# Kernel tuning notes

Measured on AMD Instinct MI355X. Metric: run time of the kernel, lower is better.

The kernel has to match this reference:

```python
import jax, jax.numpy as jnp
import numpy as np

T, B, D_IN, D_H = 1024, 128, 256, 256


def setup_inputs() -> dict:
    key = jax.random.key(0)
    ks = jax.random.split(key, 9)
    s_in = 1.0 / np.sqrt(D_IN + D_H)  # torch nn.Linear init scale
    inputs = jax.random.normal(ks[0], (T, B, D_IN), dtype=jnp.float32)
    def lin(kw, kb):
        W = jax.random.uniform(kw, (D_IN + D_H, D_H), jnp.float32, -s_in, s_in)
        b = jax.random.uniform(kb, (D_H,), jnp.float32, -s_in, s_in)
        return W, b
    Wf, bf = lin(ks[1], ks[2])
    Wi, bi = lin(ks[3], ks[4])
    Wg, bg = lin(ks[5], ks[6])
    Wo, bo = lin(ks[7], ks[8])
    return {"inputs": inputs, "Wf": Wf, "bf": bf, "Wi": Wi, "bi": bi,
            "Wg": Wg, "bg": bg, "Wo": Wo, "bo": bo}


def reference(inputs, Wf, bf, Wi, bi, Wg, bg, Wo, bo):
    Bsz = inputs.shape[1]
    h0 = jnp.zeros((Bsz, D_H), inputs.dtype)
    c0 = jnp.zeros((Bsz, D_H), inputs.dtype)

    def step(carry, x):
        hx, cx = carry
        combined = jnp.concatenate([x, hx], axis=1)  # [B, D_IN+D_H]
        f = jax.nn.sigmoid(combined @ Wf + bf)
        i = jax.nn.sigmoid(combined @ Wi + bi)
        g = jnp.tanh(combined @ Wg + bg)
        o = jax.nn.sigmoid(combined @ Wo + bo)
        cx = f * cx + i * g
        hx = o * jnp.tanh(cx)
        return (hx, cx), hx

    (hx, cx), outputs = jax.lax.scan(step, (h0, c0), inputs)
    return outputs, (hx, cx)
```

## Files before the change

### kernel.cpp

```cpp
#include <hip/hip_runtime.h>
#include <hip/hip_bf16.h>

typedef short s16x8 __attribute__((ext_vector_type(8)));
typedef int   i32x4 __attribute__((ext_vector_type(4)));
typedef float f32x4 __attribute__((ext_vector_type(4)));
typedef float f32x2 __attribute__((ext_vector_type(2)));

#define T_STEPS 1024
#define BATCH   128
#define DIN     256
#define DH      256
#define NWG     64
#define NTHREADS 256

static __device__ __forceinline__ short f2bf(float f) {
  return __builtin_bit_cast(short, (__bf16)f);
}
static __device__ __forceinline__ float sigf(float x){ return 1.f/(1.f+__expf(-x)); }
static __device__ __forceinline__ float tanhfast(float x){ return 1.f - 2.f/(1.f+__expf(2.f*x)); }

static __device__ __forceinline__ i32x4 ld16_cc(const void* p){
  i32x4 r; asm volatile("global_load_dwordx4 %0, %1, off sc0 sc1" : "=v"(r) : "v"(p) : "memory"); return r;
}
static __device__ __forceinline__ unsigned ld4_cc(const void* p){
  unsigned r; asm volatile("global_load_dword %0, %1, off sc0 sc1\ns_waitcnt vmcnt(0)" : "=v"(r) : "v"(p) : "memory"); return r;
}
static __device__ __forceinline__ void st4_cc(void* p, unsigned v){
  asm volatile("global_store_dword %0, %1, off sc0 sc1" :: "v"(p), "v"(v) : "memory");
}

static __device__ __forceinline__ s16x8 cvt8(f32x4 a, f32x4 b){
  s16x8 r;
  r[0]=f2bf(a[0]); r[1]=f2bf(a[1]); r[2]=f2bf(a[2]); r[3]=f2bf(a[3]);
  r[4]=f2bf(b[0]); r[5]=f2bf(b[1]); r[6]=f2bf(b[2]); r[7]=f2bf(b[3]);
  return r;
}

__global__ __launch_bounds__(NTHREADS, 1)
void lstm_rc(const float* __restrict__ X,
             const float* __restrict__ Wf, const float* __restrict__ bfv,
             const float* __restrict__ Wi, const float* __restrict__ biv,
             const float* __restrict__ Wg, const float* __restrict__ bgv,
             const float* __restrict__ Wo, const float* __restrict__ bov,
             float* __restrict__ out,
             unsigned short* __restrict__ hbuf,
             unsigned int* __restrict__ flags,
             int needEnd)
{
  const int bid = blockIdx.x;
  const int r   = bid & 7;
  const int csl = bid >> 3;
  const int tid = threadIdx.x;
  const int lane = tid & 63, wv = tid >> 6;
  const int grp = lane >> 4, l15 = lane & 15;
  const int r0 = r * 16;

  __shared__ short bfx[64 * 64 * 8];
  __shared__ float elds[4 * 16 * 36];

  s16x8 bh[2][8];
  {
    const float* Wm[4] = {Wf, Wi, Wg, Wo};
    const int gate = l15 >> 2, jj = l15 & 3;
    const float* Wsrc = Wm[gate];
#pragma unroll
    for (int n2 = 0; n2 < 2; ++n2) {
      const int hc = csl * 32 + (wv * 2 + n2) * 4 + jj;
#pragma unroll
      for (int kk = 0; kk < 16; ++kk) {
        const float* p = Wsrc + (size_t)(kk * 32 + grp * 8) * DH + hc;
        s16x8 f;
#pragma unroll
        for (int s = 0; s < 8; ++s) f[s] = f2bf(p[(size_t)s * DH]);
        if (kk < 8) *(s16x8*)&bfx[(((wv * 2 + n2) * 8 + kk) * 64 + lane) * 8] = f;
        else        bh[n2][kk - 8] = f;
      }
    }
  }

  const int colg = csl * 32 + wv * 8 + 2 * grp;
  float bia[4][2];
  {
    const float* Bv[4] = {bfv, biv, bgv, bov};
#pragma unroll
    for (int g = 0; g < 4; ++g) { bia[g][0] = Bv[g][colg]; bia[g][1] = Bv[g][colg + 1]; }
  }
  __syncthreads();

  f32x4 xr[16];
  {
    const float* xs0 = X + (size_t)(r0 + l15) * DIN + grp * 8;
#pragma unroll
    for (int kk = 0; kk < 8; ++kk) {
      xr[2 * kk]     = *(const f32x4*)(xs0 + kk * 32);
      xr[2 * kk + 1] = *(const f32x4*)(xs0 + kk * 32 + 4);
    }
  }
  f32x4 accx0 = {0.f,0.f,0.f,0.f}, accx1 = {0.f,0.f,0.f,0.f};
#pragma unroll
  for (int kk = 0; kk < 8; ++kk) {
    s16x8 fa = cvt8(xr[2 * kk], xr[2 * kk + 1]);
    s16x8 b0 = *(const s16x8*)&bfx[(((wv * 2 + 0) * 8 + kk) * 64 + lane) * 8];
    s16x8 b1 = *(const s16x8*)&bfx[(((wv * 2 + 1) * 8 + kk) * 64 + lane) * 8];
    accx0 = __builtin_amdgcn_mfma_f32_16x16x32_bf16(fa, b0, accx0, 0, 0, 0);
    accx1 = __builtin_amdgcn_mfma_f32_16x16x32_bf16(fa, b1, accx1, 0, 0, 0);
  }

  unsigned* myflag = flags + (r * 32 + csl);
  const unsigned* pollp = flags + (r * 32 + (lane & 7));
  float* eldsw = &elds[wv * 16 * 36];
  float cs0 = 0.f, cs1 = 0.f, h0s = 0.f, h1s = 0.f;

  for (int t = 0; t < T_STEPS; ++t) {
    while (1) {
      unsigned v = ld4_cc(pollp);
      if (__all((int)(v >= (unsigned)t))) break;
    }
    __builtin_amdgcn_sched_barrier(0);

    const unsigned short* hr = hbuf + (size_t)(t & 1) * (BATCH * DH)
                             + (size_t)(r0 + l15) * DH + grp * 8;
    i32x4 hraw[8];
#pragma unroll
    for (int q = 0; q < 8; ++q) hraw[q] = ld16_cc(hr + q * 32);
    asm volatile("s_waitcnt vmcnt(0)" ::: "memory");
    __builtin_amdgcn_sched_barrier(0);

    f32x4 acc0 = accx0, acc1 = accx1;
#pragma unroll
    for (int q = 0; q < 8; ++q) {
      s16x8 ah = __builtin_bit_cast(s16x8, hraw[q]);
      acc0 = __builtin_amdgcn_mfma_f32_16x16x32_bf16(ah, bh[0][q], acc0, 0, 0, 0);
      acc1 = __builtin_amdgcn_mfma_f32_16x16x32_bf16(ah, bh[1][q], acc1, 0, 0, 0);
    }

#pragma unroll
    for (int rr = 0; rr < 4; ++rr) {
      eldsw[(grp * 4 + rr) * 36 + l15]      = acc0[rr];
      eldsw[(grp * 4 + rr) * 36 + 16 + l15] = acc1[rr];
    }
    asm volatile("s_waitcnt lgkmcnt(0)" ::: "memory");
    __builtin_amdgcn_sched_barrier(0);
    float z0[4], z1[4];
    const int hc0 = 2 * grp, hc1 = 2 * grp + 1;
#pragma unroll
    for (int g = 0; g < 4; ++g) {
      z0[g] = eldsw[l15 * 36 + ((hc0 >> 2) << 4) + 4 * g + (hc0 & 3)];
      z1[g] = eldsw[l15 * 36 + ((hc1 >> 2) << 4) + 4 * g + (hc1 & 3)];
    }

    {
      float zf = z0[0] + bia[0][0], zi = z0[1] + bia[1][0];
      float zg = z0[2] + bia[2][0], zo = z0[3] + bia[3][0];
      cs0 = sigf(zf) * cs0 + sigf(zi) * tanhfast(zg);
      h0s = sigf(zo) * tanhfast(cs0);
    }
    {
      float zf = z1[0] + bia[0][1], zi = z1[1] + bia[1][1];
      float zg = z1[2] + bia[2][1], zo = z1[3] + bia[3][1];
      cs1 = sigf(zf) * cs1 + sigf(zi) * tanhfast(zg);
      h1s = sigf(zo) * tanhfast(cs1);
    }

    const int row = r0 + l15;
    {
      unsigned hpk = (unsigned)(unsigned short)f2bf(h0s)
                   | ((unsigned)(unsigned short)f2bf(h1s) << 16);
      st4_cc(hbuf + (size_t)((t + 1) & 1) * (BATCH * DH)
             + (size_t)row * DH + colg, hpk);
    }
    asm volatile("s_waitcnt vmcnt(0)" ::: "memory");
    __syncthreads();
    if (tid == 0) st4_cc(myflag, (unsigned)(t + 1));

    {
      f32x2 ov; ov[0] = h0s; ov[1] = h1s;
      *(f32x2*)(out + ((size_t)t * BATCH + row) * DH + colg) = ov;
    }
    {
      const int tnx = (t + 1 < T_STEPS) ? t + 1 : T_STEPS - 1;
      const float* xs = X + ((size_t)tnx * BATCH + r0 + l15) * DIN + grp * 8;
#pragma unroll
      for (int kk = 0; kk < 8; ++kk) {
        xr[2 * kk]     = *(const f32x4*)(xs + kk * 32);
        xr[2 * kk + 1] = *(const f32x4*)(xs + kk * 32 + 4);
      }
    }
    accx0 = (f32x4){0.f,0.f,0.f,0.f}; accx1 = (f32x4){0.f,0.f,0.f,0.f};
#pragma unroll
    for (int kk = 0; kk < 8; ++kk) {
      s16x8 fa = cvt8(xr[2 * kk], xr[2 * kk + 1]);
      s16x8 b0 = *(const s16x8*)&bfx[(((wv * 2 + 0) * 8 + kk) * 64 + lane) * 8];
      s16x8 b1 = *(const s16x8*)&bfx[(((wv * 2 + 1) * 8 + kk) * 64 + lane) * 8];
      accx0 = __builtin_amdgcn_mfma_f32_16x16x32_bf16(fa, b0, accx0, 0, 0, 0);
      accx1 = __builtin_amdgcn_mfma_f32_16x16x32_bf16(fa, b1, accx1, 0, 0, 0);
    }
  }

  if (needEnd) {
    if (wv == 0) {
      const unsigned* fp = flags + ((lane >> 3) * 32 + (lane & 7));
      while (ld4_cc(fp) < (unsigned)T_STEPS) __builtin_amdgcn_s_sleep(1);
    }
    __syncthreads();
  }
  {
    const size_t base = (size_t)T_STEPS * BATCH * DH;
    const size_t idx  = (size_t)(r0 + l15) * DH + colg;
    out[base + idx]     = h0s;
    out[base + idx + 1] = h1s;
    out[base + BATCH * DH + idx]     = cs0;
    out[base + BATCH * DH + idx + 1] = cs1;
  }
}

extern "C" void kernel_launch(void* const* d_in, const int* in_sizes, int n_in,
                              void* d_out, int out_size, void* d_ws, size_t ws_size,
                              hipStream_t stream) {
  const float* X   = (const float*)d_in[0];
  const float* Wf  = (const float*)d_in[1];
  const float* bf_ = (const float*)d_in[2];
  const float* Wi  = (const float*)d_in[3];
  const float* bi_ = (const float*)d_in[4];
  const float* Wg  = (const float*)d_in[5];
  const float* bg_ = (const float*)d_in[6];
  const float* Wo  = (const float*)d_in[7];
  const float* bo_ = (const float*)d_in[8];
  float* out = (float*)d_out;

  const size_t hbytes = (size_t)2 * BATCH * DH * 2;
  const size_t fbytes = 2048;
  unsigned short* hbuf;
  unsigned int*   flags;
  int needEnd;
  if (ws_size >= hbytes + fbytes) {
    hbuf  = (unsigned short*)d_ws;
    flags = (unsigned int*)((unsigned char*)d_ws + hbytes);
    needEnd = 0;
    hipMemsetAsync(d_ws, 0, hbytes + fbytes, stream);
  } else {
    unsigned char* tail = (unsigned char*)d_out + (size_t)T_STEPS * BATCH * DH * 4;
    hbuf  = (unsigned short*)tail;
    flags = (unsigned int*)(tail + hbytes);
    needEnd = 1;
    hipMemsetAsync(tail, 0, hbytes + fbytes, stream);
  }

  lstm_rc<<<NWG, NTHREADS, 0, stream>>>(X, Wf, bf_, Wi, bi_, Wg, bg_,
                                        Wo, bo_, out, hbuf, flags, needEnd);
}
```

Baseline: 4.414 ms.

## Interleave two independent batch halves per workgroup to hide cross-block sync latency

Halves the grid to 32 workgroups, each handling two 16-row batch slices (A and B) whose recurrences are independent, so the wait on one slice's flags overlaps with compute on the other. Synchronisation moves from a per-block __syncthreads plus one flag to per-wave flags polled by 32 lanes. The input projection is staged as bf16 into double-buffered LDS, with X prefetched two steps ahead. Each workgroup does twice the MFMA work per step, and the two-phase ordering adds complexity to the memory-ordering logic.

```diff
diff --git a/kernel.cpp b/kernel.cpp
--- a/kernel.cpp
+++ b/kernel.cpp
@@ -10,52 +10,57 @@
 #define BATCH   128
 #define DIN     256
 #define DH      256
-#define NWG     64
+#define NWG     32
 #define NTHREADS 256
 
-static __device__ __forceinline__ short f2bf(float f) {
-  return __builtin_bit_cast(short, (__bf16)f);
+static __device__ __forceinline__ short f2bf(float f){ return __builtin_bit_cast(short,(__bf16)f); }
+static __device__ __forceinline__ float sigf(float x){ return 1.f/(1.f+__expf(-x)); }
+static __device__ __forceinline__ float tanhfast(float x){ return 1.f-2.f/(1.f+__expf(2.f*x)); }
+
+static __device__ __forceinline__ i32x4 ld16_cc_i(const void* p){ i32x4 r; asm volatile("global_load_dwordx4 %0, %1, off sc0 sc1" : "=v"(r) : "v"(p) : "memory"); return r; }
+static __device__ __forceinline__ i32x4 ld16_pl_i(const void* p){ i32x4 r; asm volatile("global_load_dwordx4 %0, %1, off" : "=v"(r) : "v"(p) : "memory"); return r; }
+static __device__ __forceinline__ unsigned ld4_cc_i(const void* p){ unsigned r; asm volatile("global_load_dword %0, %1, off sc0 sc1" : "=v"(r) : "v"(p) : "memory"); return r; }
+static __device__ __forceinline__ unsigned ld4_cc_w(const void* p){ unsigned r; asm volatile("global_load_dword %0, %1, off sc0 sc1\ns_waitcnt vmcnt(0)" : "=v"(r) : "v"(p) : "memory"); return r; }
+static __device__ __forceinline__ void st4_cc_i(void* p, unsigned v){ asm volatile("global_store_dword %0, %1, off sc0 sc1" :: "v"(p), "v"(v) : "memory"); }
+static __device__ __forceinline__ void st8_pl_i(void* p, f32x2 v){ asm volatile("global_store_dwordx2 %0, %1, off" :: "v"(p), "v"(v) : "memory"); }
+#define VMW(n)  asm volatile("s_waitcnt vmcnt(" #n ")" ::: "memory")
+#define LGKM0   asm volatile("s_waitcnt lgkmcnt(0)" ::: "memory")
+#define SCHED0  __builtin_amdgcn_sched_barrier(0)
+#define POLLWAIT(val, ptr, tgt) \
+  while (!__all((int)((val) >= (unsigned)(tgt)))) { (val) = ld4_cc_w(ptr); }
+
+static __device__ __forceinline__ void stageX(short* dst, int xseg, int xrow,
+                                              f32x4 a, f32x4 b, f32x4 c, f32x4 d){
+  s16x8 lo, hi;
+  lo[0]=f2bf(a[0]); lo[1]=f2bf(a[1]); lo[2]=f2bf(a[2]); lo[3]=f2bf(a[3]);
+  lo[4]=f2bf(b[0]); lo[5]=f2bf(b[1]); lo[6]=f2bf(b[2]); lo[7]=f2bf(b[3]);
+  hi[0]=f2bf(c[0]); hi[1]=f2bf(c[1]); hi[2]=f2bf(c[2]); hi[3]=f2bf(c[3]);
+  hi[4]=f2bf(d[0]); hi[5]=f2bf(d[1]); hi[6]=f2bf(d[2]); hi[7]=f2bf(d[3]);
+  *(s16x8*)&dst[((2*xseg+0)*16 + xrow)*8] = lo;
+  *(s16x8*)&dst[((2*xseg+1)*16 + xrow)*8] = hi;
 }
-static __device__ __forceinline__ float sigf(float x){ return 1.f/(1.f+__expf(-x)); }
-static __device__ __forceinline__ float tanhfast(float x){ return 1.f - 2.f/(1.f+__expf(2.f*x)); }
-
-static __device__ __forceinline__ i32x4 ld16_cc(const void* p){
-  i32x4 r; asm volatile("global_load_dwordx4 %0, %1, off sc0 sc1" : "=v"(r) : "v"(p) : "memory"); return r;
-}
-static __device__ __forceinline__ unsigned ld4_cc(const void* p){
-  unsigned r; asm volatile("global_load_dword %0, %1, off sc0 sc1\ns_waitcnt vmcnt(0)" : "=v"(r) : "v"(p) : "memory"); return r;
-}
-static __device__ __forceinline__ void st4_cc(void* p, unsigned v){
-  asm volatile("global_store_dword %0, %1, off sc0 sc1" :: "v"(p), "v"(v) : "memory");
-}
-
-static __device__ __forceinline__ s16x8 cvt8(f32x4 a, f32x4 b){
-  s16x8 r;
-  r[0]=f2bf(a[0]); r[1]=f2bf(a[1]); r[2]=f2bf(a[2]); r[3]=f2bf(a[3]);
-  r[4]=f2bf(b[0]); r[5]=f2bf(b[1]); r[6]=f2bf(b[2]); r[7]=f2bf(b[3]);
-  return r;
-}
 
 __global__ __launch_bounds__(NTHREADS, 1)
-void lstm_rc(const float* __restrict__ X,
-             const float* __restrict__ Wf, const float* __restrict__ bfv,
-             const float* __restrict__ Wi, const float* __restrict__ biv,
-             const float* __restrict__ Wg, const float* __restrict__ bgv,
-             const float* __restrict__ Wo, const float* __restrict__ bov,
-             float* __restrict__ out,
-             unsigned short* __restrict__ hbuf,
-             unsigned int* __restrict__ flags,
-             int needEnd)
+void lstm_pipe(const float* __restrict__ X,
+               const float* __restrict__ Wf, const float* __restrict__ bfv,
+               const float* __restrict__ Wi, const float* __restrict__ biv,
+               const float* __restrict__ Wg, const float* __restrict__ bgv,
+               const float* __restrict__ Wo, const float* __restrict__ bov,
+               float* __restrict__ out,
+               unsigned short* __restrict__ hbuf,
+               unsigned int* __restrict__ flags,
+               int needEnd)
 {
   const int bid = blockIdx.x;
-  const int r   = bid & 7;
-  const int csl = bid >> 3;
+  const int g   = bid & 3;
+  const int csl = bid >> 2;
   const int tid = threadIdx.x;
   const int lane = tid & 63, wv = tid >> 6;
   const int grp = lane >> 4, l15 = lane & 15;
-  const int r0 = r * 16;
+  const int r0A = g * 32, r0B = g * 32 + 16;
 
   __shared__ short bfx[64 * 64 * 8];
+  __shared__ short axl[4 * 32 * 16 * 8];
   __shared__ float elds[4 * 16 * 36];
 
   s16x8 bh[2][8];
@@ -83,134 +88,225 @@
   {
     const float* Bv[4] = {bfv, biv, bgv, bov};
 #pragma unroll
-    for (int g = 0; g < 4; ++g) { bia[g][0] = Bv[g][colg]; bia[g][1] = Bv[g][colg + 1]; }
+    for (int q = 0; q < 4; ++q) { bia[q][0] = Bv[q][colg]; bia[q][1] = Bv[q][colg + 1]; }
   }
   __syncthreads();
 
-  f32x4 xr[16];
-  {
-    const float* xs0 = X + (size_t)(r0 + l15) * DIN + grp * 8;
-#pragma unroll
-    for (int kk = 0; kk < 8; ++kk) {
-      xr[2 * kk]     = *(const f32x4*)(xs0 + kk * 32);
-      xr[2 * kk + 1] = *(const f32x4*)(xs0 + kk * 32 + 4);
-    }
-  }
-  f32x4 accx0 = {0.f,0.f,0.f,0.f}, accx1 = {0.f,0.f,0.f,0.f};
-#pragma unroll
-  for (int kk = 0; kk < 8; ++kk) {
-    s16x8 fa = cvt8(xr[2 * kk], xr[2 * kk + 1]);
-    s16x8 b0 = *(const s16x8*)&bfx[(((wv * 2 + 0) * 8 + kk) * 64 + lane) * 8];
-    s16x8 b1 = *(const s16x8*)&bfx[(((wv * 2 + 1) * 8 + kk) * 64 + lane) * 8];
-    accx0 = __builtin_amdgcn_mfma_f32_16x16x32_bf16(fa, b0, accx0, 0, 0, 0);
-    accx1 = __builtin_amdgcn_mfma_f32_16x16x32_bf16(fa, b1, accx1, 0, 0, 0);
-  }
-
-  unsigned* myflag = flags + (r * 32 + csl);
-  const unsigned* pollp = flags + (r * 32 + (lane & 7));
+  const int xrow = tid & 15, xseg = tid >> 4;
+  {
+    const float* xsA = X + (size_t)(r0A + xrow) * DIN + xseg * 16;
+    stageX(axl + 0 * (32 * 16 * 8), xseg, xrow,
+           *(const f32x4*)xsA, *(const f32x4*)(xsA + 4),
+           *(const f32x4*)(xsA + 8), *(const f32x4*)(xsA + 12));
+    const float* xsB = X + (size_t)(r0B + xrow) * DIN + xseg * 16;
+    stageX(axl + 2 * (32 * 16 * 8), xseg, xrow,
+           *(const f32x4*)xsB, *(const f32x4*)(xsB + 4),
+           *(const f32x4*)(xsB + 8), *(const f32x4*)(xsB + 12));
+  }
+  __syncthreads();
+
+  const unsigned* pollA = flags + (g * 2 + 0) * 32 + (lane & 31);
+  const unsigned* pollB = flags + (g * 2 + 1) * 32 + (lane & 31);
+  unsigned* flagAw = flags + (g * 2 + 0) * 32 + csl * 4 + wv;
+  unsigned* flagBw = flags + (g * 2 + 1) * 32 + csl * 4 + wv;
   float* eldsw = &elds[wv * 16 * 36];
-  float cs0 = 0.f, cs1 = 0.f, h0s = 0.f, h1s = 0.f;
+
+  f32x4 xra[4], xrb[4];
+  {
+    const float* xs = X + ((size_t)1 * BATCH + r0A + xrow) * DIN + xseg * 16;
+    xra[0] = __builtin_bit_cast(f32x4, ld16_pl_i(xs));
+    xra[1] = __builtin_bit_cast(f32x4, ld16_pl_i(xs + 4));
+    xra[2] = __builtin_bit_cast(f32x4, ld16_pl_i(xs + 8));
+    xra[3] = __builtin_bit_cast(f32x4, ld16_pl_i(xs + 12));
+  }
+  unsigned pav = ld4_cc_i(pollA), pbv;
+  {
+    const float* xs = X + ((size_t)1 * BATCH + r0B + xrow) * DIN + xseg * 16;
+    xrb[0] = __builtin_bit_cast(f32x4, ld16_pl_i(xs));
+    xrb[1] = __builtin_bit_cast(f32x4, ld16_pl_i(xs + 4));
+    xrb[2] = __builtin_bit_cast(f32x4, ld16_pl_i(xs + 8));
+    xrb[3] = __builtin_bit_cast(f32x4, ld16_pl_i(xs + 12));
+  }
+
+  float csA0 = 0.f, csA1 = 0.f, hA0v = 0.f, hA1v = 0.f;
+  float csB0 = 0.f, csB1 = 0.f, hB0v = 0.f, hB1v = 0.f;
 
   for (int t = 0; t < T_STEPS; ++t) {
-    while (1) {
-      unsigned v = ld4_cc(pollp);
-      if (__all((int)(v >= (unsigned)t))) break;
-    }
-    __builtin_amdgcn_sched_barrier(0);
-
-    const unsigned short* hr = hbuf + (size_t)(t & 1) * (BATCH * DH)
-                             + (size_t)(r0 + l15) * DH + grp * 8;
-    i32x4 hraw[8];
-#pragma unroll
-    for (int q = 0; q < 8; ++q) hraw[q] = ld16_cc(hr + q * 32);
-    asm volatile("s_waitcnt vmcnt(0)" ::: "memory");
-    __builtin_amdgcn_sched_barrier(0);
-
-    f32x4 acc0 = accx0, acc1 = accx1;
+    const int pr = t & 1, pw = (t + 1) & 1;
+
+    VMW(4); SCHED0;
+    POLLWAIT(pav, pollA, t);
+    SCHED0;
+
+    pbv = ld4_cc_i(pollB);
+    const unsigned short* hrA = hbuf + (size_t)pr * (BATCH * DH)
+                              + (size_t)(r0A + l15) * DH + grp * 8;
+    i32x4 ha[8];
+#pragma unroll
+    for (int q = 0; q < 8; ++q) ha[q] = ld16_cc_i(hrA + q * 32);
+
+    f32x4 a0 = {0.f,0.f,0.f,0.f}, a1 = {0.f,0.f,0.f,0.f};
+    {
+      const short* ab = axl + (0 * 2 + pr) * (32 * 16 * 8);
+#pragma unroll
+      for (int kk = 0; kk < 8; ++kk) {
+        s16x8 a  = *(const s16x8*)&ab[((kk * 4 + grp) * 16 + l15) * 8];
+        s16x8 b0 = *(const s16x8*)&bfx[(((wv * 2 + 0) * 8 + kk) * 64 + lane) * 8];
+        s16x8 b1 = *(const s16x8*)&bfx[(((wv * 2 + 1) * 8 + kk) * 64 + lane) * 8];
+        a0 = __builtin_amdgcn_mfma_f32_16x16x32_bf16(a, b0, a0, 0, 0, 0);
+        a1 = __builtin_amdgcn_mfma_f32_16x16x32_bf16(a, b1, a1, 0, 0, 0);
+      }
+    }
+
+    VMW(0); SCHED0;
+    POLLWAIT(pbv, pollB, t);
+    SCHED0;
+
+    const unsigned short* hrB = hbuf + (size_t)pr * (BATCH * DH)
+                              + (size_t)(r0B + l15) * DH + grp * 8;
+    i32x4 hb[8];
+#pragma unroll
+    for (int q = 0; q < 8; ++q) hb[q] = ld16_cc_i(hrB + q * 32);
+
 #pragma unroll
     for (int q = 0; q < 8; ++q) {
-      s16x8 ah = __builtin_bit_cast(s16x8, hraw[q]);
-      acc0 = __builtin_amdgcn_mfma_f32_16x16x32_bf16(ah, bh[0][q], acc0, 0, 0, 0);
-      acc1 = __builtin_amdgcn_mfma_f32_16x16x32_bf16(ah, bh[1][q], acc1, 0, 0, 0);
+      s16x8 ah = __builtin_bit_cast(s16x8, ha[q]);
+      a0 = __builtin_amdgcn_mfma_f32_16x16x32_bf16(ah, bh[0][q], a0, 0, 0, 0);
+      a1 = __builtin_amdgcn_mfma_f32_16x16x32_bf16(ah, bh[1][q], a1, 0, 0, 0);
     }
 
 #pragma unroll
     for (int rr = 0; rr < 4; ++rr) {
-      eldsw[(grp * 4 + rr) * 36 + l15]      = acc0[rr];
-      eldsw[(grp * 4 + rr) * 36 + 16 + l15] = acc1[rr];
-    }
-    asm volatile("s_waitcnt lgkmcnt(0)" ::: "memory");
-    __builtin_amdgcn_sched_barrier(0);
-    float z0[4], z1[4];
-    const int hc0 = 2 * grp, hc1 = 2 * grp + 1;
-#pragma unroll
-    for (int g = 0; g < 4; ++g) {
-      z0[g] = eldsw[l15 * 36 + ((hc0 >> 2) << 4) + 4 * g + (hc0 & 3)];
-      z1[g] = eldsw[l15 * 36 + ((hc1 >> 2) << 4) + 4 * g + (hc1 & 3)];
-    }
-
-    {
+      eldsw[(grp * 4 + rr) * 36 + l15]      = a0[rr];
+      eldsw[(grp * 4 + rr) * 36 + 16 + l15] = a1[rr];
+    }
+    LGKM0; SCHED0;
+    {
+      const int hc0 = 2 * grp, hc1 = 2 * grp + 1;
+      float z0[4], z1[4];
+#pragma unroll
+      for (int q = 0; q < 4; ++q) {
+        z0[q] = eldsw[l15 * 36 + ((hc0 >> 2) << 4) + 4 * q + (hc0 & 3)];
+        z1[q] = eldsw[l15 * 36 + ((hc1 >> 2) << 4) + 4 * q + (hc1 & 3)];
+      }
       float zf = z0[0] + bia[0][0], zi = z0[1] + bia[1][0];
       float zg = z0[2] + bia[2][0], zo = z0[3] + bia[3][0];
-      cs0 = sigf(zf) * cs0 + sigf(zi) * tanhfast(zg);
-      h0s = sigf(zo) * tanhfast(cs0);
-    }
-    {
-      float zf = z1[0] + bia[0][1], zi = z1[1] + bia[1][1];
-      float zg = z1[2] + bia[2][1], zo = z1[3] + bia[3][1];
-      cs1 = sigf(zf) * cs1 + sigf(zi) * tanhfast(zg);
-      h1s = sigf(zo) * tanhfast(cs1);
-    }
-
-    const int row = r0 + l15;
-    {
-      unsigned hpk = (unsigned)(unsigned short)f2bf(h0s)
-                   | ((unsigned)(unsigned short)f2bf(h1s) << 16);
-      st4_cc(hbuf + (size_t)((t + 1) & 1) * (BATCH * DH)
-             + (size_t)row * DH + colg, hpk);
-    }
-    asm volatile("s_waitcnt vmcnt(0)" ::: "memory");
+      csA0 = sigf(zf) * csA0 + sigf(zi) * tanhfast(zg);
+      hA0v = sigf(zo) * tanhfast(csA0);
+      zf = z1[0] + bia[0][1]; zi = z1[1] + bia[1][1];
+      zg = z1[2] + bia[2][1]; zo = z1[3] + bia[3][1];
+      csA1 = sigf(zf) * csA1 + sigf(zi) * tanhfast(zg);
+      hA1v = sigf(zo) * tanhfast(csA1);
+    }
+
+    {
+      unsigned hpk = (unsigned)(unsigned short)f2bf(hA0v)
+                   | ((unsigned)(unsigned short)f2bf(hA1v) << 16);
+      st4_cc_i(hbuf + (size_t)pw * (BATCH * DH) + (size_t)(r0A + l15) * DH + colg, hpk);
+      f32x2 ov; ov[0] = hA0v; ov[1] = hA1v;
+      st8_pl_i(out + ((size_t)t * BATCH + (r0A + l15)) * DH + colg, ov);
+    }
+
+    stageX(axl + (0 * 2 + pw) * (32 * 16 * 8), xseg, xrow, xra[0], xra[1], xra[2], xra[3]);
+    LGKM0;
+
+    VMW(1); SCHED0;
+    if (lane == 0) st4_cc_i(flagAw, (unsigned)(t + 1));
+
+    {
+      const int tp = (t + 2 < T_STEPS) ? t + 2 : T_STEPS - 1;
+      const float* xs = X + ((size_t)tp * BATCH + r0A + xrow) * DIN + xseg * 16;
+      xra[0] = __builtin_bit_cast(f32x4, ld16_pl_i(xs));
+      xra[1] = __builtin_bit_cast(f32x4, ld16_pl_i(xs + 4));
+      xra[2] = __builtin_bit_cast(f32x4, ld16_pl_i(xs + 8));
+      xra[3] = __builtin_bit_cast(f32x4, ld16_pl_i(xs + 12));
+    }
+
+    f32x4 b0 = {0.f,0.f,0.f,0.f}, b1 = {0.f,0.f,0.f,0.f};
+    {
+      const short* ab = axl + (1 * 2 + pr) * (32 * 16 * 8);
+#pragma unroll
+      for (int kk = 0; kk < 8; ++kk) {
+        s16x8 a  = *(const s16x8*)&ab[((kk * 4 + grp) * 16 + l15) * 8];
+        s16x8 bb0 = *(const s16x8*)&bfx[(((wv * 2 + 0) * 8 + kk) * 64 + lane) * 8];
+        s16x8 bb1 = *(const s16x8*)&bfx[(((wv * 2 + 1) * 8 + kk) * 64 + lane) * 8];
+        b0 = __builtin_amdgcn_mfma_f32_16x16x32_bf16(a, bb0, b0, 0, 0, 0);
+        b1 = __builtin_amdgcn_mfma_f32_16x16x32_bf16(a, bb1, b1, 0, 0, 0);
+      }
+    }
+#pragma unroll
+    for (int q = 0; q < 8; ++q) {
+      s16x8 ah = __builtin_bit_cast(s16x8, hb[q]);
+      b0 = __builtin_amdgcn_mfma_f32_16x16x32_bf16(ah, bh[0][q], b0, 0, 0, 0);
+      b1 = __builtin_amdgcn_mfma_f32_16x16x32_bf16(ah, bh[1][q], b1, 0, 0, 0);
+    }
+
+#pragma unroll
+    for (int rr = 0; rr < 4; ++rr) {
+      eldsw[(grp * 4 + rr) * 36 + l15]      = b0[rr];
+      eldsw[(grp * 4 + rr) * 36 + 16 + l15] = b1[rr];
+    }
+    LGKM0; SCHED0;
+    {
+      const int hc0 = 2 * grp, hc1 = 2 * grp + 1;
+      float z0[4], z1[4];
+#pragma unroll
+      for (int q = 0; q < 4; ++q) {
+        z0[q] = eldsw[l15 * 36 + ((hc0 >> 2) << 4) + 4 * q + (hc0 & 3)];
+        z1[q] = eldsw[l15 * 36 + ((hc1 >> 2) << 4) + 4 * q + (hc1 & 3)];
+      }
+      float zf = z0[0] + bia[0][0], zi = z0[1] + bia[1][0];
+      float zg = z0[2] + bia[2][0], zo = z0[3] + bia[3][0];
+      csB0 = sigf(zf) * csB0 + sigf(zi) * tanhfast(zg);
+      hB0v = sigf(zo) * tanhfast(csB0);
+      zf = z1[0] + bia[0][1]; zi = z1[1] + bia[1][1];
+      zg = z1[2] + bia[2][1]; zo = z1[3] + bia[3][1];
+      csB1 = sigf(zf) * csB1 + sigf(zi) * tanhfast(zg);
+      hB1v = sigf(zo) * tanhfast(csB1);
+    }
+
+    {
+      unsigned hpk = (unsigned)(unsigned short)f2bf(hB0v)
+                   | ((unsigned)(unsigned short)f2bf(hB1v) << 16);
+      st4_cc_i(hbuf + (size_t)pw * (BATCH * DH) + (size_t)(r0B + l15) * DH + colg, hpk);
+      f32x2 ov; ov[0] = hB0v; ov[1] = hB1v;
+      st8_pl_i(out + ((size_t)t * BATCH + (r0B + l15)) * DH + colg, ov);
+    }
+
+    stageX(axl + (1 * 2 + pw) * (32 * 16 * 8), xseg, xrow, xrb[0], xrb[1], xrb[2], xrb[3]);
+    LGKM0;
+
+    VMW(1); SCHED0;
+    if (lane == 0) st4_cc_i(flagBw, (unsigned)(t + 1));
+
+    pav = ld4_cc_i(pollA);
+    {
+      const int tp = (t + 2 < T_STEPS) ? t + 2 : T_STEPS - 1;
+      const float* xs = X + ((size_t)tp * BATCH + r0B + xrow) * DIN + xseg * 16;
+      xrb[0] = __builtin_bit_cast(f32x4, ld16_pl_i(xs));
+      xrb[1] = __builtin_bit_cast(f32x4, ld16_pl_i(xs + 4));
+      xrb[2] = __builtin_bit_cast(f32x4, ld16_pl_i(xs + 8));
+      xrb[3] = __builtin_bit_cast(f32x4, ld16_pl_i(xs + 12));
+    }
+  }
+
+  if (needEnd) {
+    const unsigned* fp = flags + tid;
+    while (ld4_cc_w(fp) < (unsigned)T_STEPS) __builtin_amdgcn_s_sleep(1);
     __syncthreads();
-    if (tid == 0) st4_cc(myflag, (unsigned)(t + 1));
-
-    {
-      f32x2 ov; ov[0] = h0s; ov[1] = h1s;
-      *(f32x2*)(out + ((size_t)t * BATCH + row) * DH + colg) = ov;
-    }
-    {
-      const int tnx = (t + 1 < T_STEPS) ? t + 1 : T_STEPS - 1;
-      const float* xs = X + ((size_t)tnx * BATCH + r0 + l15) * DIN + grp * 8;
-#pragma unroll
-      for (int kk = 0; kk < 8; ++kk) {
-        xr[2 * kk]     = *(const f32x4*)(xs + kk * 32);
-        xr[2 * kk + 1] = *(const f32x4*)(xs + kk * 32 + 4);
-      }
-    }
-    accx0 = (f32x4){0.f,0.f,0.f,0.f}; accx1 = (f32x4){0.f,0.f,0.f,0.f};
-#pragma unroll
-    for (int kk = 0; kk < 8; ++kk) {
-      s16x8 fa = cvt8(xr[2 * kk], xr[2 * kk + 1]);
-      s16x8 b0 = *(const s16x8*)&bfx[(((wv * 2 + 0) * 8 + kk) * 64 + lane) * 8];
-      s16x8 b1 = *(const s16x8*)&bfx[(((wv * 2 + 1) * 8 + kk) * 64 + lane) * 8];
-      accx0 = __builtin_amdgcn_mfma_f32_16x16x32_bf16(fa, b0, accx0, 0, 0, 0);
-      accx1 = __builtin_amdgcn_mfma_f32_16x16x32_bf16(fa, b1, accx1, 0, 0, 0);
-    }
-  }
-
-  if (needEnd) {
-    if (wv == 0) {
-      const unsigned* fp = flags + ((lane >> 3) * 32 + (lane & 7));
-      while (ld4_cc(fp) < (unsigned)T_STEPS) __builtin_amdgcn_s_sleep(1);
-    }
-    __syncthreads();
   }
   {
     const size_t base = (size_t)T_STEPS * BATCH * DH;
-    const size_t idx  = (size_t)(r0 + l15) * DH + colg;
-    out[base + idx]     = h0s;
-    out[base + idx + 1] = h1s;
-    out[base + BATCH * DH + idx]     = cs0;
-    out[base + BATCH * DH + idx + 1] = cs1;
+    const size_t idxA = (size_t)(r0A + l15) * DH + colg;
+    const size_t idxB = (size_t)(r0B + l15) * DH + colg;
+    out[base + idxA]     = hA0v;
+    out[base + idxA + 1] = hA1v;
+    out[base + BATCH * DH + idxA]     = csA0;
+    out[base + BATCH * DH + idxA + 1] = csA1;
+    out[base + idxB]     = hB0v;
+    out[base + idxB + 1] = hB1v;
+    out[base + BATCH * DH + idxB]     = csB0;
+    out[base + BATCH * DH + idxB + 1] = csB1;
   }
 }
 
@@ -246,6 +342,6 @@
     hipMemsetAsync(tail, 0, hbytes + fbytes, stream);
   }
 
-  lstm_rc<<<NWG, NTHREADS, 0, stream>>>(X, Wf, bf_, Wi, bi_, Wg, bg_,
-                                        Wo, bo_, out, hbuf, flags, needEnd);
+  lstm_pipe<<<NWG, NTHREADS, 0, stream>>>(X, Wf, bf_, Wi, bi_, Wg, bg_,
+                                          Wo, bo_, out, hbuf, flags, needEnd);
 }
```

Measured after the change: 4.261 ms. 1.04x faster.

## Split LSTM batch across independent workgroups streaming prepacked bf16 weights

Applied to the files above, without the earlier changes.

Replaces the 64-workgroup kernel, which synchronises every timestep through global flags, with 16 independent workgroups of 512 threads. Each workgroup owns 8 batch rows and keeps h and x in LDS, so no cross-workgroup synchronisation is needed. Weights are prepacked once into MFMA fragment layout in bf16 by a separate kernel. Every timestep then streams all weights (1 MB per workgroup) from L2/global through a triple-buffered register pipeline. This trades inter-WG flag latency for heavy repeated weight bandwidth, and only half of each 16-row MFMA tile holds real batch rows. The new path is used only when the workspace is at least 1 MB.

```diff
diff --git a/kernel.cpp b/kernel.cpp
--- a/kernel.cpp
+++ b/kernel.cpp
@@ -2,6 +2,7 @@
 #include <hip/hip_bf16.h>
 
 typedef short s16x8 __attribute__((ext_vector_type(8)));
+typedef short s16x4 __attribute__((ext_vector_type(4)));
 typedef int   i32x4 __attribute__((ext_vector_type(4)));
 typedef float f32x4 __attribute__((ext_vector_type(4)));
 typedef float f32x2 __attribute__((ext_vector_type(2)));
@@ -10,14 +11,190 @@
 #define BATCH   128
 #define DIN     256
 #define DH      256
-#define NWG     64
-#define NTHREADS 256
-
-static __device__ __forceinline__ short f2bf(float f) {
-  return __builtin_bit_cast(short, (__bf16)f);
-}
+
+static __device__ __forceinline__ short f2bf(float f){ return __builtin_bit_cast(short,(__bf16)f); }
 static __device__ __forceinline__ float sigf(float x){ return 1.f/(1.f+__expf(-x)); }
-static __device__ __forceinline__ float tanhfast(float x){ return 1.f - 2.f/(1.f+__expf(2.f*x)); }
+static __device__ __forceinline__ float tanhfast(float x){ return 1.f-2.f/(1.f+__expf(2.f*x)); }
+
+__global__ void build_frags(const float* __restrict__ Wf, const float* __restrict__ Wi,
+                            const float* __restrict__ Wg, const float* __restrict__ Wo,
+                            unsigned short* __restrict__ frag) {
+  const float* Wm[4] = {Wf, Wi, Wg, Wo};
+  int p0 = blockIdx.x * 256 + threadIdx.x;
+#pragma unroll
+  for (int i = 0; i < 4; ++i) {
+    int p = p0 + i * 16384;
+    int lane = p & 63;
+    int F = p >> 6;
+    int kk = F & 15, gate = (F >> 4) & 3, b = (F >> 6) & 1, w = F >> 7;
+    int k0 = kk * 32 + (lane >> 4) * 8;
+    int col = w * 32 + b * 16 + (lane & 15);
+    const float* src = Wm[gate] + (size_t)k0 * DH + col;
+    unsigned short* dst = frag + (size_t)p * 8;
+#pragma unroll
+    for (int s = 0; s < 8; ++s) dst[s] = (unsigned short)f2bf(src[(size_t)s * DH]);
+  }
+}
+
+#define LDF(dst, base, OFF) \
+  asm volatile("global_load_dwordx4 %0, %1, off offset:" #OFF : "=v"(dst) : "v"(base) : "memory")
+#define WAITV(N) do { asm volatile("s_waitcnt vmcnt(" #N ")" ::: "memory"); \
+  __builtin_amdgcn_sched_barrier(0); } while (0)
+
+#define HALF_ISSUE(B) do { \
+  LDF(bq[B][0], fwp, 0); LDF(bq[B][1], fwp, 1024); \
+  LDF(bq[B][2], fwp, 2048); LDF(bq[B][3], fwp, 3072); \
+  LDF(bq[B][4], fwp2, 0); LDF(bq[B][5], fwp2, 1024); \
+  LDF(bq[B][6], fwp2, 2048); LDF(bq[B][7], fwp2, 3072); \
+  fwp += 8192; fwp2 += 8192; } while (0)
+
+#define HALF_MFMA(B, AARR, BI, GI) do { \
+  acc[BI][GI] = __builtin_amdgcn_mfma_f32_16x16x32_bf16(AARR[0], __builtin_bit_cast(s16x8, bq[B][0]), acc[BI][GI], 0,0,0); \
+  acc[BI][GI] = __builtin_amdgcn_mfma_f32_16x16x32_bf16(AARR[1], __builtin_bit_cast(s16x8, bq[B][1]), acc[BI][GI], 0,0,0); \
+  acc[BI][GI] = __builtin_amdgcn_mfma_f32_16x16x32_bf16(AARR[2], __builtin_bit_cast(s16x8, bq[B][2]), acc[BI][GI], 0,0,0); \
+  acc[BI][GI] = __builtin_amdgcn_mfma_f32_16x16x32_bf16(AARR[3], __builtin_bit_cast(s16x8, bq[B][3]), acc[BI][GI], 0,0,0); \
+  acc[BI][GI] = __builtin_amdgcn_mfma_f32_16x16x32_bf16(AARR[4], __builtin_bit_cast(s16x8, bq[B][4]), acc[BI][GI], 0,0,0); \
+  acc[BI][GI] = __builtin_amdgcn_mfma_f32_16x16x32_bf16(AARR[5], __builtin_bit_cast(s16x8, bq[B][5]), acc[BI][GI], 0,0,0); \
+  acc[BI][GI] = __builtin_amdgcn_mfma_f32_16x16x32_bf16(AARR[6], __builtin_bit_cast(s16x8, bq[B][6]), acc[BI][GI], 0,0,0); \
+  acc[BI][GI] = __builtin_amdgcn_mfma_f32_16x16x32_bf16(AARR[7], __builtin_bit_cast(s16x8, bq[B][7]), acc[BI][GI], 0,0,0); } while (0)
+
+#define EPI(BI, CBX) do { \
+  _Pragma("unroll") \
+  for (int r = 0; r < 4; ++r) { \
+    float zf = acc[BI][0][r] + bia[0][BI]; \
+    float zi = acc[BI][1][r] + bia[1][BI]; \
+    float zg = acc[BI][2][r] + bia[2][BI]; \
+    float zo = acc[BI][3][r] + bia[3][BI]; \
+    float cn = sigf(zf) * cs[BI][r] + sigf(zi) * tanhfast(zg); \
+    cs[BI][r] = cn; \
+    float hv = sigf(zo) * tanhfast(cn); \
+    hq[BI][r] = hv; \
+    if (grp < 2) HL[pw * 4352 + (grp * 4 + r) * 272 + (CBX)] = (unsigned short)f2bf(hv); \
+  } } while (0)
+
+__global__ __launch_bounds__(512, 2)
+void lstm_cu(const float* __restrict__ X,
+             const float* __restrict__ bfv, const float* __restrict__ biv,
+             const float* __restrict__ bgv, const float* __restrict__ bov,
+             const unsigned short* __restrict__ frag,
+             float* __restrict__ out)
+{
+  const int tid = threadIdx.x;
+  const int lane = tid & 63, w = tid >> 6;
+  const int grp = lane >> 4, l15 = lane & 15;
+  const int g8 = blockIdx.x * 8;
+
+  __shared__ unsigned short XL[2 * 16 * 272];
+  __shared__ unsigned short HL[2 * 16 * 272];
+
+  for (int i = tid; i < 2 * 16 * 272; i += 512) { XL[i] = 0; HL[i] = 0; }
+
+  const int cb0 = w * 32 + l15, cb1 = w * 32 + 16 + l15;
+  float bia[4][2];
+  {
+    const float* Bv[4] = {bfv, biv, bgv, bov};
+#pragma unroll
+    for (int g = 0; g < 4; ++g) { bia[g][0] = Bv[g][cb0]; bia[g][1] = Bv[g][cb1]; }
+  }
+
+  const int xr = tid >> 6, xc = (tid & 63) * 4;
+
+  {
+    f32x4 v = *(const f32x4*)(X + ((size_t)0 * BATCH + g8 + xr) * DIN + xc);
+    s16x4 h4; h4[0]=f2bf(v[0]); h4[1]=f2bf(v[1]); h4[2]=f2bf(v[2]); h4[3]=f2bf(v[3]);
+    *(s16x4*)&XL[0 * 4352 + xr * 272 + xc] = h4;
+  }
+  __syncthreads();
+
+  i32x4 xq;
+  LDF(xq, (const char*)(X + ((size_t)1 * BATCH + g8 + xr) * DIN + xc), 0);
+
+  const char* fragw = (const char*)frag + (size_t)w * 131072;
+  float cs[2][4] = {{0,0,0,0},{0,0,0,0}};
+  float hq[2][4] = {{0,0,0,0},{0,0,0,0}};
+
+  for (int t = 0; t < T_STEPS; ++t) {
+    const int pr = t & 1, pw = pr ^ 1;
+
+    asm volatile("s_waitcnt vmcnt(0)" ::: "memory");
+    __builtin_amdgcn_sched_barrier(0);
+
+    {
+      f32x4 v = __builtin_bit_cast(f32x4, xq);
+      s16x4 h4; h4[0]=f2bf(v[0]); h4[1]=f2bf(v[1]); h4[2]=f2bf(v[2]); h4[3]=f2bf(v[3]);
+      *(s16x4*)&XL[pw * 4352 + xr * 272 + xc] = h4;
+    }
+
+    s16x8 ax[8], ah[8];
+#pragma unroll
+    for (int q = 0; q < 8; ++q) {
+      ax[q] = *(const s16x8*)&XL[pr * 4352 + l15 * 272 + q * 32 + grp * 8];
+      ah[q] = *(const s16x8*)&HL[pr * 4352 + l15 * 272 + q * 32 + grp * 8];
+    }
+
+    f32x4 acc[2][4];
+#pragma unroll
+    for (int b = 0; b < 2; ++b)
+#pragma unroll
+      for (int g = 0; g < 4; ++g) acc[b][g] = (f32x4){0.f,0.f,0.f,0.f};
+
+    i32x4 bq[3][8];
+    const char* fwp  = fragw + lane * 16;
+    const char* fwp2 = fwp + 4096;
+
+    HALF_ISSUE(0); HALF_ISSUE(1);
+    HALF_ISSUE(2); WAITV(16); HALF_MFMA(0, ax, 0, 0);
+    HALF_ISSUE(0); WAITV(16); HALF_MFMA(1, ah, 0, 0);
+    HALF_ISSUE(1); WAITV(16); HALF_MFMA(2, ax, 0, 1);
+    HALF_ISSUE(2); WAITV(16); HALF_MFMA(0, ah, 0, 1);
+    HALF_ISSUE(0); WAITV(16); HALF_MFMA(1, ax, 0, 2);
+    HALF_ISSUE(1); WAITV(16); HALF_MFMA(2, ah, 0, 2);
+    HALF_ISSUE(2); WAITV(16); HALF_MFMA(0, ax, 0, 3);
+    HALF_ISSUE(0); WAITV(16); HALF_MFMA(1, ah, 0, 3);
+    EPI(0, cb0);
+    HALF_ISSUE(1); WAITV(16); HALF_MFMA(2, ax, 1, 0);
+    HALF_ISSUE(2); WAITV(16); HALF_MFMA(0, ah, 1, 0);
+    HALF_ISSUE(0); WAITV(16); HALF_MFMA(1, ax, 1, 1);
+    HALF_ISSUE(1); WAITV(16); HALF_MFMA(2, ah, 1, 1);
+    HALF_ISSUE(2); WAITV(16); HALF_MFMA(0, ax, 1, 2);
+    HALF_ISSUE(0); WAITV(16); HALF_MFMA(1, ah, 1, 2);
+    WAITV(8);  HALF_MFMA(2, ax, 1, 3);
+    WAITV(0);  HALF_MFMA(0, ah, 1, 3);
+
+    {
+      const int tp = (t + 2 < T_STEPS) ? t + 2 : T_STEPS - 1;
+      LDF(xq, (const char*)(X + ((size_t)tp * BATCH + g8 + xr) * DIN + xc), 0);
+    }
+
+    EPI(1, cb1);
+
+    if (grp < 2) {
+      size_t rb = ((size_t)t * BATCH + g8 + grp * 4) * DH;
+#pragma unroll
+      for (int r = 0; r < 4; ++r) {
+        out[rb + (size_t)r * DH + cb0] = hq[0][r];
+        out[rb + (size_t)r * DH + cb1] = hq[1][r];
+      }
+    }
+
+    asm volatile("s_waitcnt lgkmcnt(0)" ::: "memory");
+    __builtin_amdgcn_sched_barrier(0);
+    __builtin_amdgcn_s_barrier();
+    __builtin_amdgcn_sched_barrier(0);
+  }
+
+  if (grp < 2) {
+    const size_t base = (size_t)T_STEPS * BATCH * DH;
+#pragma unroll
+    for (int r = 0; r < 4; ++r) {
+      size_t idx = (size_t)(g8 + grp * 4 + r) * DH;
+      out[base + idx + cb0] = hq[0][r];
+      out[base + idx + cb1] = hq[1][r];
+      out[base + BATCH * DH + idx + cb0] = cs[0][r];
+      out[base + BATCH * DH + idx + cb1] = cs[1][r];
+    }
+  }
+}
 
 static __device__ __forceinline__ i32x4 ld16_cc(const void* p){
   i32x4 r; asm volatile("global_load_dwordx4 %0, %1, off sc0 sc1" : "=v"(r) : "v"(p) : "memory"); return r;
@@ -28,7 +205,6 @@
 static __device__ __forceinline__ void st4_cc(void* p, unsigned v){
   asm volatile("global_store_dword %0, %1, off sc0 sc1" :: "v"(p), "v"(v) : "memory");
 }
-
 static __device__ __forceinline__ s16x8 cvt8(f32x4 a, f32x4 b){
   s16x8 r;
   r[0]=f2bf(a[0]); r[1]=f2bf(a[1]); r[2]=f2bf(a[2]); r[3]=f2bf(a[3]);
@@ -36,16 +212,16 @@
   return r;
 }
 
-__global__ __launch_bounds__(NTHREADS, 1)
-void lstm_rc(const float* __restrict__ X,
-             const float* __restrict__ Wf, const float* __restrict__ bfv,
-             const float* __restrict__ Wi, const float* __restrict__ biv,
-             const float* __restrict__ Wg, const float* __restrict__ bgv,
-             const float* __restrict__ Wo, const float* __restrict__ bov,
-             float* __restrict__ out,
-             unsigned short* __restrict__ hbuf,
-             unsigned int* __restrict__ flags,
-             int needEnd)
+__global__ __launch_bounds__(256, 1)
+void lstm_rc_fb(const float* __restrict__ X,
+                const float* __restrict__ Wf, const float* __restrict__ bfv,
+                const float* __restrict__ Wi, const float* __restrict__ biv,
+                const float* __restrict__ Wg, const float* __restrict__ bgv,
+                const float* __restrict__ Wo, const float* __restrict__ bov,
+                float* __restrict__ out,
+                unsigned short* __restrict__ hbuf,
+                unsigned int* __restrict__ flags,
+                int needEnd)
 {
   const int bid = blockIdx.x;
   const int r   = bid & 7;
@@ -148,7 +324,6 @@
       z0[g] = eldsw[l15 * 36 + ((hc0 >> 2) << 4) + 4 * g + (hc0 & 3)];
       z1[g] = eldsw[l15 * 36 + ((hc1 >> 2) << 4) + 4 * g + (hc1 & 3)];
     }
-
     {
       float zf = z0[0] + bia[0][0], zi = z0[1] + bia[1][0];
       float zg = z0[2] + bia[2][0], zo = z0[3] + bia[3][0];
@@ -161,7 +336,6 @@
       cs1 = sigf(zf) * cs1 + sigf(zi) * tanhfast(zg);
       h1s = sigf(zo) * tanhfast(cs1);
     }
-
     const int row = r0 + l15;
     {
       unsigned hpk = (unsigned)(unsigned short)f2bf(h0s)
@@ -227,6 +401,13 @@
   const float* Wo  = (const float*)d_in[7];
   const float* bo_ = (const float*)d_in[8];
   float* out = (float*)d_out;
+
+  if (ws_size >= (size_t)(1u << 20)) {
+    unsigned short* frag = (unsigned short*)d_ws;
+    build_frags<<<64, 256, 0, stream>>>(Wf, Wi, Wg, Wo, frag);
+    lstm_cu<<<16, 512, 0, stream>>>(X, bf_, bi_, bg_, bo_, frag, out);
+    return;
+  }
 
   const size_t hbytes = (size_t)2 * BATCH * DH * 2;
   const size_t fbytes = 2048;
@@ -245,7 +426,6 @@
     needEnd = 1;
     hipMemsetAsync(tail, 0, hbytes + fbytes, stream);
   }
-
-  lstm_rc<<<NWG, NTHREADS, 0, stream>>>(X, Wf, bf_, Wi, bi_, Wg, bg_,
-                                        Wo, bo_, out, hbuf, flags, needEnd);
-}
+  lstm_rc_fb<<<64, 256, 0, stream>>>(X, Wf, bf_, Wi, bi_, Wg, bg_,
+                                     Wo, bo_, out, hbuf, flags, needEnd);
+}
```

Measured after the change: 12.57 ms. 2.85x slower.

## Replace flag polling with timestep-tagged hidden-state words for inter-block sync

Applied to the files above, without the earlier changes.

Each bf16 hidden value is now stored in a 32-bit word whose upper half carries the timestep tag. Consumers poll the hidden-state data directly until every tag matches the current step. This removes the separate flag write, the vmcnt wait plus __syncthreads before publishing, and the flag-then-data double round trip on the per-step critical path. In exchange each step reads twice as many bytes and retries full loads while spinning, and the old flag path is kept as a fallback when the workspace is too small.

```diff
diff --git a/kernel.cpp b/kernel.cpp
--- a/kernel.cpp
+++ b/kernel.cpp
@@ -3,6 +3,7 @@
 
 typedef short s16x8 __attribute__((ext_vector_type(8)));
 typedef int   i32x4 __attribute__((ext_vector_type(4)));
+typedef unsigned u32x2 __attribute__((ext_vector_type(2)));
 typedef float f32x4 __attribute__((ext_vector_type(4)));
 typedef float f32x2 __attribute__((ext_vector_type(2)));
 
@@ -13,11 +14,9 @@
 #define NWG     64
 #define NTHREADS 256
 
-static __device__ __forceinline__ short f2bf(float f) {
-  return __builtin_bit_cast(short, (__bf16)f);
-}
+static __device__ __forceinline__ short f2bf(float f){ return __builtin_bit_cast(short,(__bf16)f); }
 static __device__ __forceinline__ float sigf(float x){ return 1.f/(1.f+__expf(-x)); }
-static __device__ __forceinline__ float tanhfast(float x){ return 1.f - 2.f/(1.f+__expf(2.f*x)); }
+static __device__ __forceinline__ float tanhfast(float x){ return 1.f-2.f/(1.f+__expf(2.f*x)); }
 
 static __device__ __forceinline__ i32x4 ld16_cc(const void* p){
   i32x4 r; asm volatile("global_load_dwordx4 %0, %1, off sc0 sc1" : "=v"(r) : "v"(p) : "memory"); return r;
@@ -27,6 +26,9 @@
 }
 static __device__ __forceinline__ void st4_cc(void* p, unsigned v){
   asm volatile("global_store_dword %0, %1, off sc0 sc1" :: "v"(p), "v"(v) : "memory");
+}
+static __device__ __forceinline__ void st8_cc(void* p, u32x2 v){
+  asm volatile("global_store_dwordx2 %0, %1, off sc0 sc1" :: "v"(p), "v"(v) : "memory");
 }
 
 static __device__ __forceinline__ s16x8 cvt8(f32x4 a, f32x4 b){
@@ -37,15 +39,13 @@
 }
 
 __global__ __launch_bounds__(NTHREADS, 1)
-void lstm_rc(const float* __restrict__ X,
-             const float* __restrict__ Wf, const float* __restrict__ bfv,
-             const float* __restrict__ Wi, const float* __restrict__ biv,
-             const float* __restrict__ Wg, const float* __restrict__ bgv,
-             const float* __restrict__ Wo, const float* __restrict__ bov,
-             float* __restrict__ out,
-             unsigned short* __restrict__ hbuf,
-             unsigned int* __restrict__ flags,
-             int needEnd)
+void lstm_tag(const float* __restrict__ X,
+              const float* __restrict__ Wf, const float* __restrict__ bfv,
+              const float* __restrict__ Wi, const float* __restrict__ biv,
+              const float* __restrict__ Wg, const float* __restrict__ bgv,
+              const float* __restrict__ Wo, const float* __restrict__ bov,
+              float* __restrict__ out,
+              unsigned* __restrict__ htag)
 {
   const int bid = blockIdx.x;
   const int r   = bid & 7;
@@ -106,6 +106,187 @@
     accx1 = __builtin_amdgcn_mfma_f32_16x16x32_bf16(fa, b1, accx1, 0, 0, 0);
   }
 
+  float cs0 = 0.f, cs1 = 0.f, h0s = 0.f, h1s = 0.f;
+
+  for (int t = 0; t < T_STEPS; ++t) {
+    const unsigned tte = (unsigned)t << 16;
+    const unsigned* hb = htag + (size_t)(t & 1) * (BATCH * DH)
+                       + (size_t)(r0 + l15) * DH + grp * 8;
+    i32x4 hraw[16];
+    while (1) {
+#pragma unroll
+      for (int q = 0; q < 8; ++q) {
+        hraw[2 * q]     = ld16_cc(hb + q * 32);
+        hraw[2 * q + 1] = ld16_cc(hb + q * 32 + 4);
+      }
+      asm volatile("s_waitcnt vmcnt(0)" ::: "memory");
+      unsigned bad = 0;
+#pragma unroll
+      for (int i2 = 0; i2 < 16; ++i2)
+        bad |= (unsigned)(hraw[i2][0] ^ (int)tte) | (unsigned)(hraw[i2][2] ^ (int)tte);
+      bad &= 0xFFFF0000u;
+      if (__all((int)(bad == 0))) break;
+    }
+    __builtin_amdgcn_sched_barrier(0);
+
+    f32x4 acc0 = accx0, acc1 = accx1;
+#pragma unroll
+    for (int q = 0; q < 8; ++q) {
+      i32x4 hp;
+      hp[0] = (int)__builtin_amdgcn_perm((unsigned)hraw[2*q][1],   (unsigned)hraw[2*q][0],   0x05040100u);
+      hp[1] = (int)__builtin_amdgcn_perm((unsigned)hraw[2*q][3],   (unsigned)hraw[2*q][2],   0x05040100u);
+      hp[2] = (int)__builtin_amdgcn_perm((unsigned)hraw[2*q+1][1], (unsigned)hraw[2*q+1][0], 0x05040100u);
+      hp[3] = (int)__builtin_amdgcn_perm((unsigned)hraw[2*q+1][3], (unsigned)hraw[2*q+1][2], 0x05040100u);
+      s16x8 ah = __builtin_bit_cast(s16x8, hp);
+      acc0 = __builtin_amdgcn_mfma_f32_16x16x32_bf16(ah, bh[0][q], acc0, 0, 0, 0);
+      acc1 = __builtin_amdgcn_mfma_f32_16x16x32_bf16(ah, bh[1][q], acc1, 0, 0, 0);
+    }
+
+#pragma unroll
+    for (int rr = 0; rr < 4; ++rr) {
+      float* eldsw = &elds[wv * 16 * 36];
+      eldsw[(grp * 4 + rr) * 36 + l15]      = acc0[rr];
+      eldsw[(grp * 4 + rr) * 36 + 16 + l15] = acc1[rr];
+    }
+    asm volatile("s_waitcnt lgkmcnt(0)" ::: "memory");
+    __builtin_amdgcn_sched_barrier(0);
+    float z0[4], z1[4];
+    {
+      const float* eldsw = &elds[wv * 16 * 36];
+      const int hc0 = 2 * grp, hc1 = 2 * grp + 1;
+#pragma unroll
+      for (int g = 0; g < 4; ++g) {
+        z0[g] = eldsw[l15 * 36 + ((hc0 >> 2) << 4) + 4 * g + (hc0 & 3)];
+        z1[g] = eldsw[l15 * 36 + ((hc1 >> 2) << 4) + 4 * g + (hc1 & 3)];
+      }
+    }
+
+    {
+      float zf = z0[0] + bia[0][0], zi = z0[1] + bia[1][0];
+      float zg = z0[2] + bia[2][0], zo = z0[3] + bia[3][0];
+      cs0 = sigf(zf) * cs0 + sigf(zi) * tanhfast(zg);
+      h0s = sigf(zo) * tanhfast(cs0);
+    }
+    {
+      float zf = z1[0] + bia[0][1], zi = z1[1] + bia[1][1];
+      float zg = z1[2] + bia[2][1], zo = z1[3] + bia[3][1];
+      cs1 = sigf(zf) * cs1 + sigf(zi) * tanhfast(zg);
+      h1s = sigf(zo) * tanhfast(cs1);
+    }
+
+    const int row = r0 + l15;
+    {
+      const unsigned ttw = (unsigned)(t + 1) << 16;
+      u32x2 hpk;
+      hpk[0] = (unsigned)(unsigned short)f2bf(h0s) | ttw;
+      hpk[1] = (unsigned)(unsigned short)f2bf(h1s) | ttw;
+      st8_cc(htag + (size_t)((t + 1) & 1) * (BATCH * DH) + (size_t)row * DH + colg, hpk);
+    }
+
+    {
+      f32x2 ov; ov[0] = h0s; ov[1] = h1s;
+      *(f32x2*)(out + ((size_t)t * BATCH + row) * DH + colg) = ov;
+    }
+    {
+      const int tnx = (t + 1 < T_STEPS) ? t + 1 : T_STEPS - 1;
+      const float* xs = X + ((size_t)tnx * BATCH + r0 + l15) * DIN + grp * 8;
+#pragma unroll
+      for (int kk = 0; kk < 8; ++kk) {
+        xr[2 * kk]     = *(const f32x4*)(xs + kk * 32);
+        xr[2 * kk + 1] = *(const f32x4*)(xs + kk * 32 + 4);
+      }
+    }
+    accx0 = (f32x4){0.f,0.f,0.f,0.f}; accx1 = (f32x4){0.f,0.f,0.f,0.f};
+#pragma unroll
+    for (int kk = 0; kk < 8; ++kk) {
+      s16x8 fa = cvt8(xr[2 * kk], xr[2 * kk + 1]);
+      s16x8 b0 = *(const s16x8*)&bfx[(((wv * 2 + 0) * 8 + kk) * 64 + lane) * 8];
+      s16x8 b1 = *(const s16x8*)&bfx[(((wv * 2 + 1) * 8 + kk) * 64 + lane) * 8];
+      accx0 = __builtin_amdgcn_mfma_f32_16x16x32_bf16(fa, b0, accx0, 0, 0, 0);
+      accx1 = __builtin_amdgcn_mfma_f32_16x16x32_bf16(fa, b1, accx1, 0, 0, 0);
+    }
+  }
+
+  {
+    const size_t base = (size_t)T_STEPS * BATCH * DH;
+    const size_t idx  = (size_t)(r0 + l15) * DH + colg;
+    out[base + idx]     = h0s;
+    out[base + idx + 1] = h1s;
+    out[base + BATCH * DH + idx]     = cs0;
+    out[base + BATCH * DH + idx + 1] = cs1;
+  }
+}
+
+__global__ __launch_bounds__(NTHREADS, 1)
+void lstm_rc_fb(const float* __restrict__ X,
+                const float* __restrict__ Wf, const float* __restrict__ bfv,
+                const float* __restrict__ Wi, const float* __restrict__ biv,
+                const float* __restrict__ Wg, const float* __restrict__ bgv,
+                const float* __restrict__ Wo, const float* __restrict__ bov,
+                float* __restrict__ out,
+                unsigned short* __restrict__ hbuf,
+                unsigned int* __restrict__ flags,
+                int needEnd)
+{
+  const int bid = blockIdx.x;
+  const int r   = bid & 7;
+  const int csl = bid >> 3;
+  const int tid = threadIdx.x;
+  const int lane = tid & 63, wv = tid >> 6;
+  const int grp = lane >> 4, l15 = lane & 15;
+  const int r0 = r * 16;
+
+  __shared__ short bfx[64 * 64 * 8];
+  __shared__ float elds[4 * 16 * 36];
+
+  s16x8 bh[2][8];
+  {
+    const float* Wm[4] = {Wf, Wi, Wg, Wo};
+    const int gate = l15 >> 2, jj = l15 & 3;
+    const float* Wsrc = Wm[gate];
+#pragma unroll
+    for (int n2 = 0; n2 < 2; ++n2) {
+      const int hc = csl * 32 + (wv * 2 + n2) * 4 + jj;
+#pragma unroll
+      for (int kk = 0; kk < 16; ++kk) {
+        const float* p = Wsrc + (size_t)(kk * 32 + grp * 8) * DH + hc;
+        s16x8 f;
+#pragma unroll
+        for (int s = 0; s < 8; ++s) f[s] = f2bf(p[(size_t)s * DH]);
+        if (kk < 8) *(s16x8*)&bfx[(((wv * 2 + n2) * 8 + kk) * 64 + lane) * 8] = f;
+        else        bh[n2][kk - 8] = f;
+      }
+    }
+  }
+
+  const int colg = csl * 32 + wv * 8 + 2 * grp;
+  float bia[4][2];
+  {
+    const float* Bv[4] = {bfv, biv, bgv, bov};
+#pragma unroll
+    for (int g = 0; g < 4; ++g) { bia[g][0] = Bv[g][colg]; bia[g][1] = Bv[g][colg + 1]; }
+  }
+  __syncthreads();
+
+  f32x4 xr[16];
+  {
+    const float* xs0 = X + (size_t)(r0 + l15) * DIN + grp * 8;
+#pragma unroll
+    for (int kk = 0; kk < 8; ++kk) {
+      xr[2 * kk]     = *(const f32x4*)(xs0 + kk * 32);
+      xr[2 * kk + 1] = *(const f32x4*)(xs0 + kk * 32 + 4);
+    }
+  }
+  f32x4 accx0 = {0.f,0.f,0.f,0.f}, accx1 = {0.f,0.f,0.f,0.f};
+#pragma unroll
+  for (int kk = 0; kk < 8; ++kk) {
+    s16x8 fa = cvt8(xr[2 * kk], xr[2 * kk + 1]);
+    s16x8 b0 = *(const s16x8*)&bfx[(((wv * 2 + 0) * 8 + kk) * 64 + lane) * 8];
+    s16x8 b1 = *(const s16x8*)&bfx[(((wv * 2 + 1) * 8 + kk) * 64 + lane) * 8];
+    accx0 = __builtin_amdgcn_mfma_f32_16x16x32_bf16(fa, b0, accx0, 0, 0, 0);
+    accx1 = __builtin_amdgcn_mfma_f32_16x16x32_bf16(fa, b1, accx1, 0, 0, 0);
+  }
+
   unsigned* myflag = flags + (r * 32 + csl);
   const unsigned* pollp = flags + (r * 32 + (lane & 7));
   float* eldsw = &elds[wv * 16 * 36];
@@ -148,7 +329,6 @@
       z0[g] = eldsw[l15 * 36 + ((hc0 >> 2) << 4) + 4 * g + (hc0 & 3)];
       z1[g] = eldsw[l15 * 36 + ((hc1 >> 2) << 4) + 4 * g + (hc1 & 3)];
     }
-
     {
       float zf = z0[0] + bia[0][0], zi = z0[1] + bia[1][0];
       float zg = z0[2] + bia[2][0], zo = z0[3] + bia[3][0];
@@ -161,7 +341,6 @@
       cs1 = sigf(zf) * cs1 + sigf(zi) * tanhfast(zg);
       h1s = sigf(zo) * tanhfast(cs1);
     }
-
     const int row = r0 + l15;
     {
       unsigned hpk = (unsigned)(unsigned short)f2bf(h0s)
@@ -228,24 +407,21 @@
   const float* bo_ = (const float*)d_in[8];
   float* out = (float*)d_out;
 
+  const size_t tagbytes = (size_t)2 * BATCH * DH * 4;
+  if (ws_size >= tagbytes) {
+    unsigned* htag = (unsigned*)d_ws;
+    hipMemsetAsync(d_ws, 0, tagbytes, stream);
+    lstm_tag<<<NWG, NTHREADS, 0, stream>>>(X, Wf, bf_, Wi, bi_, Wg, bg_,
+                                           Wo, bo_, out, htag);
+    return;
+  }
+
   const size_t hbytes = (size_t)2 * BATCH * DH * 2;
   const size_t fbytes = 2048;
-  unsigned short* hbuf;
-  unsigned int*   flags;
-  int needEnd;
-  if (ws_size >= hbytes + fbytes) {
-    hbuf  = (unsigned short*)d_ws;
-    flags = (unsigned int*)((unsigned char*)d_ws + hbytes);
-    needEnd = 0;
-    hipMemsetAsync(d_ws, 0, hbytes + fbytes, stream);
-  } else {
-    unsigned char* tail = (unsigned char*)d_out + (size_t)T_STEPS * BATCH * DH * 4;
-    hbuf  = (unsigned short*)tail;
-    flags = (unsigned int*)(tail + hbytes);
-    needEnd = 1;
-    hipMemsetAsync(tail, 0, hbytes + fbytes, stream);
-  }
-
-  lstm_rc<<<NWG, NTHREADS, 0, stream>>>(X, Wf, bf_, Wi, bi_, Wg, bg_,
-                                        Wo, bo_, out, hbuf, flags, needEnd);
-}
+  unsigned char* tail = (unsigned char*)d_out + (size_t)T_STEPS * BATCH * DH * 4;
+  unsigned short* hbuf = (unsigned short*)tail;
+  unsigned int* flags  = (unsigned int*)(tail + hbytes);
+  hipMemsetAsync(tail, 0, hbytes + fbytes, stream);
+  lstm_rc_fb<<<NWG, NTHREADS, 0, stream>>>(X, Wf, bf_, Wi, bi_, Wg, bg_,
+                                           Wo, bo_, out, hbuf, flags, 1);
+}
```

After: 4.923 ms. 1.12x slower.
